# Optimization experiments

Hardware: AMD Instinct MI355X
Metric: run time of the kernel (lower is better)

Reference implementation:

```python
import jax, jax.numpy as jnp
import numpy as np

H, W = 48, 48
MAXDIM = 1


def _build_complex(Hh, Ww):
    # Regular grid triangulation (each cell split along its anti-diagonal),
    # matching scipy Delaunay on a grid up to arbitrary diagonal tie-breaking.
    r, c = np.meshgrid(np.arange(Hh), np.arange(Ww), indexing="ij")
    v = (r * Ww + c).astype(np.int32)
    he = np.stack([v[:, :-1].ravel(), v[:, 1:].ravel()], 1)      # horizontal
    ve = np.stack([v[:-1, :].ravel(), v[1:, :].ravel()], 1)      # vertical
    de = np.stack([v[:-1, 1:].ravel(), v[1:, :-1].ravel()], 1)   # anti-diagonal (v01,v10)
    edges = np.concatenate([he, ve, de], 0).astype(np.int32)
    nh, nv = he.shape[0], ve.shape[0]
    he_id = lambda rr, cc: rr * (Ww - 1) + cc
    ve_id = lambda rr, cc: nh + rr * Ww + cc
    de_id = lambda rr, cc: nh + nv + rr * (Ww - 1) + cc
    rr, cc = np.meshgrid(np.arange(Hh - 1), np.arange(Ww - 1), indexing="ij")
    rr, cc = rr.ravel(), cc.ravel()
    triA = np.stack([he_id(rr, cc), ve_id(rr, cc), de_id(rr, cc)], 1)
    triB = np.stack([de_id(rr, cc), ve_id(rr, cc + 1), he_id(rr + 1, cc)], 1)
    tri_edges = np.concatenate([triA, triB], 0).astype(np.int32)
    return edges, tri_edges


def setup_inputs() -> dict:
    key = jax.random.key(0)
    img = jax.random.normal(key, (H, W), dtype=jnp.float32)
    edges, tri_edges = _build_complex(H, W)
    return {"img": img, "edges": jnp.asarray(edges), "tri_edges": jnp.asarray(tri_edges)}


def _filtration(img, edges, tri_edges):
    # Sublevel-set filtration: simplex value = max over its vertices.
    f = img.reshape(-1)
    fe = jnp.max(f[edges], axis=1)          # (E,)
    ft = jnp.max(fe[tri_edges], axis=1)     # (F,) max of edge maxes == max of vertices
    return jnp.concatenate([f, fe, ft])     # (m,)


@jax.jit
def _pairing(vals, edges, tri_edges):
    # Standard persistence boundary-matrix reduction over Z/2.
    E, F = edges.shape[0], tri_edges.shape[0]
    m = vals.shape[0]
    N = m - E - F
    dims = jnp.concatenate([jnp.zeros(N, jnp.int32), jnp.ones(E, jnp.int32), jnp.full((F,), 2, jnp.int32)])
    order = jnp.lexsort((dims, vals))                  # value-primary, dim tiebreak -> faces before cofaces
    rank = jnp.zeros(m, jnp.int32).at[order].set(jnp.arange(m, dtype=jnp.int32))
    R = jnp.zeros((m, m), dtype=bool)
    ecol = rank[N + jnp.arange(E)]
    R = R.at[rank[edges[:, 0]], ecol].set(True).at[rank[edges[:, 1]], ecol].set(True)
    tcol = rank[N + E + jnp.arange(F)]
    for k in range(3):
        R = R.at[rank[N + tri_edges[:, k]], tcol].set(True)
    idx = jnp.arange(m, dtype=jnp.int32)
    low = lambda col: jnp.max(jnp.where(col, idx, -1))

    def body(j, state):
        Rm, piv = state
        def cond(s):
            Rr, p = s
            l = low(Rr[:, j])
            return (l >= 0) & (p[l] >= 0)
        def step(s):
            Rr, p = s
            l = low(Rr[:, j])
            return Rr.at[:, j].set(Rr[:, j] ^ Rr[:, p[l]]), p
        Rm, piv = jax.lax.while_loop(cond, step, (Rm, piv))
        l = low(Rm[:, j])
        piv = jax.lax.cond(l >= 0, lambda p: p.at[l].set(jnp.int32(j)), lambda p: p, piv)
        return Rm, piv

    R, piv = jax.lax.fori_loop(0, m, body, (R, -jnp.ones(m, jnp.int32)))
    lowR = jnp.max(jnp.where(R, idx[:, None], -1), axis=0)
    return order, piv, lowR, dims[order]


def _diagrams(vals, order, pivot, lowR, dims_sorted, maxdim):
    vs = vals[order]
    fmax = jnp.max(vals)                      # finite death for essential classes
    paired = pivot >= 0                       # rows that are paired births
    death_paired = vs[jnp.clip(pivot, 0)]
    essential = (lowR < 0) & (pivot < 0)      # positive, never killed
    dgms = []
    for d in range(maxdim + 1):
        pd = paired & (dims_sorted == d)
        ed = essential & (dims_sorted == d)
        birth = jnp.where(pd | ed, vs, 0.0)
        death = jnp.where(pd, death_paired, 0.0) + jnp.where(ed, fmax, 0.0)
        dgms.append(jnp.stack([birth, death], axis=-1))
    return jnp.stack(dgms)                    # (maxdim+1, m, 2), zero-padded


def reference(img, edges, tri_edges):
    vals = _filtration(img, edges, tri_edges)
    order, pivot, lowR, dims_sorted = _pairing(vals, edges, tri_edges)
    return _diagrams(vals, order, pivot, lowR, dims_sorted, MAXDIM)
```

## Files before the change

kernel.cpp:

```cpp
#include <hip/hip_runtime.h>
#include <stdint.h>
#include <math.h>

typedef unsigned long long u64;

#define FMAXC 4418
#define KRANGES 128
#define BLK 1024
#define TSZ 1024
#define PSTR 1056

static __device__ __forceinline__ uint32_t f2ord(float f) {
  uint32_t u = __float_as_uint(f);
  return (u & 0x80000000u) ? ~u : (u | 0x80000000u);
}

static __device__ __forceinline__ u64 shfl_xor_u64(u64 x, int msk) {
  int lo = __shfl_xor((int)(uint32_t)x, msk, 64);
  int hi = __shfl_xor((int)(uint32_t)(x >> 32), msk, 64);
  return ((u64)(uint32_t)hi << 32) | (uint32_t)lo;
}

static __device__ __forceinline__ void edge_ab(int e, int W, int nh, int nv,
                                               int* a, int* b) {
  if (e < nh) {
    int r = e / (W - 1), c = e - r * (W - 1);
    *a = r * W + c; *b = *a + 1;
  } else if (e < nh + nv) {
    int q = e - nh;
    int r = q / W, c = q - r * W;
    *a = r * W + c; *b = *a + W;
  } else {
    int q = e - nh - nv;
    int r = q / (W - 1), c = q - r * (W - 1);
    *a = r * W + c + 1; *b = (r + 1) * W + c;
  }
}

static __device__ __forceinline__ void edge_tri(int e, int W, int H, int nh, int nv,
                                                int FH, int* tA, int* tB) {
  if (e < nh) {
    int r = e / (W - 1), c = e - r * (W - 1);
    *tA = (r <= H - 2) ? r * (W - 1) + c : -1;
    *tB = (r >= 1) ? FH + (r - 1) * (W - 1) + c : -1;
  } else if (e < nh + nv) {
    int q = e - nh;
    int r = q / W, c = q - r * W;
    *tA = (c <= W - 2) ? r * (W - 1) + c : -1;
    *tB = (c >= 1) ? FH + r * (W - 1) + (c - 1) : -1;
  } else {
    int q = e - nh - nv;
    int r = q / (W - 1), c = q - r * (W - 1);
    *tA = r * (W - 1) + c;
    *tB = FH + r * (W - 1) + c;
  }
}

static __device__ __forceinline__ int rep(volatile int* par, int v) {
  int p = par[v];
  if (p == v) return v;
  int gp = par[p];
  while (p != gp) {
    par[v] = gp;
    v = p; p = gp; gp = par[p];
  }
  return p;
}

static __device__ __forceinline__ void hook(volatile int* vp, uint32_t ab) {
  int va = (int)(ab >> 16), vb = (int)(ab & 0xffffu);
  int pa = vp[va], pb = vp[vb];
  int ga = vp[pa], gb = vp[pb];
  while (pa != ga || pb != gb) {
    if (pa != ga) { vp[va] = ga; va = pa; pa = ga; ga = vp[pa]; }
    if (pb != gb) { vp[vb] = gb; vb = pb; pb = gb; gb = vp[pb]; }
  }
  int u = pa, w = pb;
  while (u != w) {
    if (u < w) { int t = u; u = w; w = t; }
    int old = atomicCAS((int*)&vp[u], u, w);
    if (old == u) break;
    u = rep(vp, old);
    w = rep(vp, w);
  }
}

__global__ __launch_bounds__(BLK) void k_prep(
    const float* img, float* vals, u64* keys, u64* tilesorted, uint32_t* pfx,
    uint32_t* pack, float* out, int N, int E, int F, int m, int W, int H,
    int nh, int nv, int FH, int out_n, int NT) {
  __shared__ __align__(16) u64 s[TSZ];
  __shared__ uint32_t wsum[16];
  int tid = threadIdx.x, bid = blockIdx.x;
  int lane = tid & 63, wid = tid >> 6;
  int gi = bid * BLK + tid;
  for (int i = gi; i < out_n; i += NT * BLK) out[i] = 0.0f;
  if (gi < m) pack[gi] = 0u;
  int base = bid * TSZ;
  int lim = min(TSZ, m - base);
  u64 v = ~0ull;
  if (gi < m) {
    float val;
    int i = gi;
    if (i < N) {
      val = img[i];
    } else if (i < N + E) {
      int a, b;
      edge_ab(i - N, W, nh, nv, &a, &b);
      val = fmaxf(img[a], img[b]);
    } else {
      int t = i - N - E;
      if (t < FH) {
        int r = t / (W - 1), c = t - r * (W - 1);
        int bse = r * W + c;
        val = fmaxf(img[bse], fmaxf(img[bse + 1], img[bse + W]));
      } else {
        int q = t - FH;
        int r = q / (W - 1), c = q - r * (W - 1);
        int bse = r * W + c;
        val = fmaxf(img[bse + 1], fmaxf(img[bse + W], img[bse + W + 1]));
      }
    }
    vals[i] = val;
    v = ((u64)f2ord(val) << 32) | (u64)(uint32_t)i;
    keys[i] = v;
  }
  for (int k = 2; k <= TSZ; k <<= 1) {
    for (int j = k >> 1; j > 0; j >>= 1) {
      bool asc = ((tid & k) == 0);
      if (j >= 64) {
        s[tid] = v;
        __syncthreads();
        u64 u = s[tid ^ j];
        bool takeMin = (((tid & j) == 0) == asc);
        v = takeMin ? (v < u ? v : u) : (v > u ? v : u);
        __syncthreads();
      } else {
        u64 u = shfl_xor_u64(v, j);
        bool takeMin = (((tid & j) == 0) == asc);
        v = takeMin ? (v < u ? v : u) : (v > u ? v : u);
      }
    }
  }
  tilesorted[base + tid] = v;
  uint32_t v0 = 0;
  if (tid < lim) {
    int idx = (int)(v & 0xffffffffu);
    v0 = (idx < N) ? 1u : (idx < N + E ? (1u << 16) : 0u);
  }
  uint32_t sv = v0;
  #pragma unroll
  for (int off = 1; off < 64; off <<= 1) {
    uint32_t t = (uint32_t)__shfl_up((int)sv, off, 64);
    if (lane >= off) sv += t;
  }
  if (lane == 63) wsum[wid] = sv;
  __syncthreads();
  if (tid < 16) {
    uint32_t t = wsum[tid];
    #pragma unroll
    for (int off = 1; off < 16; off <<= 1) {
      uint32_t u2 = (uint32_t)__shfl_up((int)t, off, 64);
      if (tid >= off) t += u2;
    }
    wsum[tid] = t;
  }
  __syncthreads();
  uint32_t incl = sv + (wid > 0 ? wsum[wid - 1] : 0u);
  pfx[bid * PSTR + tid] = incl - v0;
  if (tid == TSZ - 1) pfx[bid * PSTR + TSZ] = incl;
}

__global__ __launch_bounds__(BLK) void k_count(
    const u64* keys, const u64* ts, const uint32_t* pfx, uint32_t* pack,
    int N, int E, int m) {
  __shared__ __align__(16) u64 s[TSZ];
  __shared__ uint32_t sp[TSZ + 1];
  int tid = threadIdx.x;
  int t = blockIdx.x;
  s[tid] = ts[(t << 10) + tid];
  sp[tid] = pfx[t * PSTR + tid];
  if (tid == 0) sp[TSZ] = pfx[t * PSTR + TSZ];
  __syncthreads();
  int ki = blockIdx.y * BLK + tid;
  if (ki >= m) return;
  u64 k0 = keys[ki];
  int cls0 = (ki < N) ? 0 : (ki < N + E ? 1 : 2);
  int lo = 0;
  #pragma unroll
  for (int step = TSZ >> 1; step >= 1; step >>= 1) {
    if (s[lo + step - 1] < k0) lo += step;
  }
  lo += (s[lo] < k0) ? 1 : 0;
  uint32_t p = sp[lo];
  uint32_t c0 = p & 0xffffu, c1 = p >> 16;
  uint32_t cc = (cls0 == 0) ? c0 : (cls0 == 1 ? c1 : (uint32_t)lo - c0 - c1);
  atomicAdd(&pack[ki], (cc << 16) | (uint32_t)lo);
}

__global__ __launch_bounds__(256) void k_maps(
    const uint32_t* pack, const float* vals,
    float* vsorted, int* vr_to_rank, int* er_to_rank, int* noderank1,
    uint32_t* eAB0, uint32_t* eAB1,
    int N, int E, int F, int m, int W, int H, int nh, int nv, int FH) {
  int i = blockIdx.x * blockDim.x + threadIdx.x;
  if (i >= m) return;
  uint32_t pk = pack[i];
  int rank = (int)(pk & 0xffffu);
  int cls = (int)(pk >> 16);
  vsorted[rank] = vals[i];
  if (i < N) {
    vr_to_rank[cls] = rank;
  } else if (i < N + E) {
    int e = i - N, er = cls;
    er_to_rank[er] = rank;
    int a, b;
    edge_ab(e, W, nh, nv, &a, &b);
    uint32_t va = pack[a] >> 16, vb = pack[b] >> 16;
    eAB0[er] = (va << 16) | vb;
    int tA, tB;
    edge_tri(e, W, H, nh, nv, FH, &tA, &tB);
    uint32_t na = (tA >= 0) ? ((uint32_t)F - (pack[N + E + tA] >> 16)) : 0u;
    uint32_t nb = (tB >= 0) ? ((uint32_t)F - (pack[N + E + tB] >> 16)) : 0u;
    eAB1[E - 1 - er] = (na << 16) | nb;
  } else {
    noderank1[F - cls] = rank;
  }
}

__global__ __launch_bounds__(BLK) void k_pair(
    const uint32_t* eAB0, const uint32_t* eAB1,
    const int* vr_to_rank, const int* er_to_rank, const int* noderank1,
    const float* vsorted, float* out, int N, int E, int F, int C, int m) {
  __shared__ __align__(16) int s_par[2 * (FMAXC + 1)];
  __shared__ uint32_t s_rc[64];
  __shared__ int s_ci[64];
  __shared__ int2 s_pairs[64];
  __shared__ int s_cnt[2];
  int tid = threadIdx.x, bid = blockIdx.x;
  int g = bid >> 7;
  int r = bid & (KRANGES - 1);
  int NODES = (g == 0) ? N : (F + 1);
  const uint32_t* eAB = (g == 0) ? eAB0 : eAB1;
  int P = r * C;
  if (P >= E) return;
  int hi = min(P + C, E);
  int nR = hi - P;
  int n1 = (nR + 1) >> 1;
  int n2 = nR - n1;
  int Q = P + n1;
  int* par1 = s_par;
  int* par2 = s_par + (FMAXC + 1);
  volatile int* vp1 = par1;
  volatile int* vp2 = par2;
  for (int x = tid; x < NODES; x += BLK) par1[x] = x;
  __syncthreads();
  for (int i = tid; i < P; i += BLK) hook(vp1, eAB[i]);
  __syncthreads();
  for (int x = tid; x < NODES; x += BLK) {
    int r0 = x;
    while (vp1[r0] != r0) r0 = vp1[r0];
    par1[x] = r0;
  }
  __syncthreads();
  for (int x = tid; x < NODES; x += BLK) par2[x] = par1[x];
  __syncthreads();
  for (int i = tid; i < n1; i += BLK) hook(vp2, eAB[P + i]);
  __syncthreads();
  for (int x = tid; x < NODES; x += BLK) {
    int r0 = x;
    while (vp2[r0] != r0) r0 = vp2[r0];
    par2[x] = r0;
  }
  __syncthreads();
  for (int q = tid; q < nR; q += BLK) {
    int sub = (q >= n1);
    int qq = sub ? q - n1 : q;
    uint32_t ab = eAB[(sub ? Q : P) + qq];
    const int* par = sub ? par2 : par1;
    int ra = par[ab >> 16], rb = par[ab & 0xffffu];
    s_rc[sub * 32 + qq] = ((uint32_t)ra << 16) | (uint32_t)rb;
  }
  __syncthreads();
  if (tid < 128) {
    int sub = tid >> 6;
    int lane = tid & 63;
    int nC = sub ? n2 : n1;
    int ebase = sub ? Q : P;
    uint32_t* rc = s_rc + sub * 32;
    int* ci = s_ci + sub * 32;
    int* par = sub ? par2 : par1;
    uint32_t rr = (lane < nC) ? rc[lane] : 0u;
    int keep = (lane < nC) && ((rr >> 16) != (rr & 0xffffu));
    u64 mask = __ballot(keep);
    if (keep) {
      int idx = __popcll(mask & ((1ull << lane) - 1ull));
      rc[idx] = rr;
      ci[idx] = lane;
    }
    int kc = __popcll(mask);
    if (lane == 0) {
      int c = 0;
      for (int i = 0; i < kc; ++i) {
        uint32_t rr2 = rc[i];
        int x = (int)(rr2 >> 16), y = (int)(rr2 & 0xffffu);
        while (par[x] != x) { par[x] = par[par[x]]; x = par[x]; }
        while (par[y] != y) { par[y] = par[par[y]]; y = par[y]; }
        if (x != y) {
          int die = x > y ? x : y, sur = x < y ? x : y;
          par[die] = sur;
          s_pairs[sub * 32 + c] = make_int2(die, ebase + ci[i]);
          c++;
        }
      }
      s_cnt[sub] = c;
    }
  }
  __syncthreads();
  int c0 = s_cnt[0], c1 = s_cnt[1];
  if (g == 0) {
    for (int q = tid; q < c0 + c1; q += BLK) {
      int2 pq = s_pairs[q < c0 ? q : 32 + (q - c0)];
      int b = vr_to_rank[pq.x], d = er_to_rank[pq.y];
      out[2 * b] = vsorted[b];
      out[2 * b + 1] = vsorted[d];
    }
    if (r == 0 && tid == 0) {
      out[0] = vsorted[0];
      out[1] = vsorted[m - 1];
    }
  } else {
    float* o1 = out + 2 * (size_t)m;
    for (int q = tid; q < c0 + c1; q += BLK) {
      int2 pq = s_pairs[q < c0 ? q : 32 + (q - c0)];
      int er = E - 1 - pq.y;
      int b = er_to_rank[er], d = noderank1[pq.x];
      o1[2 * b] = vsorted[b];
      o1[2 * b + 1] = vsorted[d];
    }
  }
}

extern "C" void kernel_launch(void* const* d_in, const int* in_sizes, int n_in,
                              void* d_out, int out_size, void* d_ws, size_t ws_size,
                              hipStream_t stream) {
  const float* img = (const float*)d_in[0];
  int N = in_sizes[0];
  int E = in_sizes[1] / 2;
  int F = in_sizes[2] / 3;
  int m = N + E + F;
  int C = (E + KRANGES - 1) / KRANGES;
  int W = (int)(sqrt((double)N) + 0.5);
  int H = N / W;
  int nh = H * (W - 1);
  int nv = (H - 1) * W;
  int FH = (H - 1) * (W - 1);
  int NT = (m + TSZ - 1) / TSZ;
  float* out = (float*)d_out;

  char* p = (char*)d_ws;
  auto alloc = [&](size_t bytes) { char* r = p; p += (bytes + 255) & ~(size_t)255; return r; };
  u64* keys        = (u64*)alloc((size_t)NT * TSZ * 8);
  u64* tilesorted  = (u64*)alloc((size_t)NT * TSZ * 8);
  uint32_t* pfx    = (uint32_t*)alloc((size_t)NT * PSTR * 4);
  float* vals      = (float*)alloc((size_t)m * 4);
  float* vsorted   = (float*)alloc((size_t)m * 4);
  uint32_t* pack   = (uint32_t*)alloc((size_t)m * 4);
  int* vr_to_rank  = (int*)alloc((size_t)N * 4);
  int* er_to_rank  = (int*)alloc((size_t)E * 4);
  int* noderank1   = (int*)alloc((size_t)(F + 1) * 4);
  uint32_t* eAB0   = (uint32_t*)alloc((size_t)E * 4);
  uint32_t* eAB1   = (uint32_t*)alloc((size_t)E * 4);
  (void)ws_size; (void)n_in;

  k_prep<<<NT, BLK, 0, stream>>>(img, vals, keys, tilesorted, pfx, pack, out,
                                 N, E, F, m, W, H, nh, nv, FH, out_size, NT);
  dim3 cg(NT, NT);
  k_count<<<cg, BLK, 0, stream>>>(keys, tilesorted, pfx, pack, N, E, m);
  k_maps<<<(m + 255) / 256, 256, 0, stream>>>(pack, vals, vsorted,
                                              vr_to_rank, er_to_rank, noderank1,
                                              eAB0, eAB1, N, E, F, m, W, H, nh, nv, FH);
  k_pair<<<2 * KRANGES, BLK, 0, stream>>>(eAB0, eAB1, vr_to_rank, er_to_rank,
                                          noderank1, vsorted, out, N, E, F, C, m);
}
```

Measured before the change: 45.67 us.

## Double the pairing blocks with single union-find per block; double-buffer sort smem

The pairing kernel previously split each of 128 edge ranges into two halves within one block, which needed two union-find arrays. It now launches 256 ranges, one per block, each using a single shared union-find array. Each block still rebuilds the prefix forest from scratch, so total redundant hooking work roughly doubles while per-block shared memory halves. The bitonic tile sort also gains a double-buffered shared array, which drops one barrier per shared-memory step, and a barrier is added before the warp-sum write.

Result: no change. 45.26 us, median of 2 (-0.9%).

```diff
diff --git a/kernel.cpp b/kernel.cpp
--- a/kernel.cpp
+++ b/kernel.cpp
@@ -5,7 +5,7 @@
 typedef unsigned long long u64;
 
 #define FMAXC 4418
-#define KRANGES 128
+#define KRANGES 256
 #define BLK 1024
 #define TSZ 1024
 #define PSTR 1056
@@ -89,7 +89,7 @@
     const float* img, float* vals, u64* keys, u64* tilesorted, uint32_t* pfx,
     uint32_t* pack, float* out, int N, int E, int F, int m, int W, int H,
     int nh, int nv, int FH, int out_n, int NT) {
-  __shared__ __align__(16) u64 s[TSZ];
+  __shared__ __align__(16) u64 s[2][TSZ];
   __shared__ uint32_t wsum[16];
   int tid = threadIdx.x, bid = blockIdx.x;
   int lane = tid & 63, wid = tid >> 6;
@@ -125,21 +125,21 @@
     v = ((u64)f2ord(val) << 32) | (u64)(uint32_t)i;
     keys[i] = v;
   }
+  int cur = 0;
   for (int k = 2; k <= TSZ; k <<= 1) {
     for (int j = k >> 1; j > 0; j >>= 1) {
       bool asc = ((tid & k) == 0);
+      bool takeMin = (((tid & j) == 0) == asc);
+      u64 u;
       if (j >= 64) {
-        s[tid] = v;
+        s[cur][tid] = v;
         __syncthreads();
-        u64 u = s[tid ^ j];
-        bool takeMin = (((tid & j) == 0) == asc);
-        v = takeMin ? (v < u ? v : u) : (v > u ? v : u);
-        __syncthreads();
+        u = s[cur][tid ^ j];
+        cur ^= 1;
       } else {
-        u64 u = shfl_xor_u64(v, j);
-        bool takeMin = (((tid & j) == 0) == asc);
-        v = takeMin ? (v < u ? v : u) : (v > u ? v : u);
+        u = shfl_xor_u64(v, j);
       }
+      v = takeMin ? (v < u ? v : u) : (v > u ? v : u);
     }
   }
   tilesorted[base + tid] = v;
@@ -154,6 +154,7 @@
     uint32_t t = (uint32_t)__shfl_up((int)sv, off, 64);
     if (lane >= off) sv += t;
   }
+  __syncthreads();
   if (lane == 63) wsum[wid] = sv;
   __syncthreads();
   if (tid < 16) {
@@ -232,13 +233,13 @@
     const uint32_t* eAB0, const uint32_t* eAB1,
     const int* vr_to_rank, const int* er_to_rank, const int* noderank1,
     const float* vsorted, float* out, int N, int E, int F, int C, int m) {
-  __shared__ __align__(16) int s_par[2 * (FMAXC + 1)];
+  __shared__ __align__(16) int s_par[FMAXC + 1];
   __shared__ uint32_t s_rc[64];
   __shared__ int s_ci[64];
   __shared__ int2 s_pairs[64];
-  __shared__ int s_cnt[2];
+  __shared__ int s_cnt;
   int tid = threadIdx.x, bid = blockIdx.x;
-  int g = bid >> 7;
+  int g = bid >> 8;
   int r = bid & (KRANGES - 1);
   int NODES = (g == 0) ? N : (F + 1);
   const uint32_t* eAB = (g == 0) ? eAB0 : eAB1;
@@ -246,81 +247,54 @@
   if (P >= E) return;
   int hi = min(P + C, E);
   int nR = hi - P;
-  int n1 = (nR + 1) >> 1;
-  int n2 = nR - n1;
-  int Q = P + n1;
-  int* par1 = s_par;
-  int* par2 = s_par + (FMAXC + 1);
-  volatile int* vp1 = par1;
-  volatile int* vp2 = par2;
-  for (int x = tid; x < NODES; x += BLK) par1[x] = x;
-  __syncthreads();
-  for (int i = tid; i < P; i += BLK) hook(vp1, eAB[i]);
+  volatile int* vp = s_par;
+  for (int x = tid; x < NODES; x += BLK) s_par[x] = x;
+  __syncthreads();
+  for (int i = tid; i < P; i += BLK) hook(vp, eAB[i]);
   __syncthreads();
   for (int x = tid; x < NODES; x += BLK) {
     int r0 = x;
-    while (vp1[r0] != r0) r0 = vp1[r0];
-    par1[x] = r0;
-  }
-  __syncthreads();
-  for (int x = tid; x < NODES; x += BLK) par2[x] = par1[x];
-  __syncthreads();
-  for (int i = tid; i < n1; i += BLK) hook(vp2, eAB[P + i]);
-  __syncthreads();
-  for (int x = tid; x < NODES; x += BLK) {
-    int r0 = x;
-    while (vp2[r0] != r0) r0 = vp2[r0];
-    par2[x] = r0;
+    while (vp[r0] != r0) r0 = vp[r0];
+    s_par[x] = r0;
   }
   __syncthreads();
   for (int q = tid; q < nR; q += BLK) {
-    int sub = (q >= n1);
-    int qq = sub ? q - n1 : q;
-    uint32_t ab = eAB[(sub ? Q : P) + qq];
-    const int* par = sub ? par2 : par1;
-    int ra = par[ab >> 16], rb = par[ab & 0xffffu];
-    s_rc[sub * 32 + qq] = ((uint32_t)ra << 16) | (uint32_t)rb;
-  }
-  __syncthreads();
-  if (tid < 128) {
-    int sub = tid >> 6;
-    int lane = tid & 63;
-    int nC = sub ? n2 : n1;
-    int ebase = sub ? Q : P;
-    uint32_t* rc = s_rc + sub * 32;
-    int* ci = s_ci + sub * 32;
-    int* par = sub ? par2 : par1;
-    uint32_t rr = (lane < nC) ? rc[lane] : 0u;
-    int keep = (lane < nC) && ((rr >> 16) != (rr & 0xffffu));
+    uint32_t ab = eAB[P + q];
+    int ra = s_par[ab >> 16], rb = s_par[ab & 0xffffu];
+    s_rc[q] = ((uint32_t)ra << 16) | (uint32_t)rb;
+  }
+  __syncthreads();
+  if (tid < 64) {
+    uint32_t rr = (tid < nR) ? s_rc[tid] : 0u;
+    int keep = (tid < nR) && ((rr >> 16) != (rr & 0xffffu));
     u64 mask = __ballot(keep);
     if (keep) {
-      int idx = __popcll(mask & ((1ull << lane) - 1ull));
-      rc[idx] = rr;
-      ci[idx] = lane;
+      int idx = __popcll(mask & ((1ull << tid) - 1ull));
+      s_rc[idx] = rr;
+      s_ci[idx] = tid;
     }
     int kc = __popcll(mask);
-    if (lane == 0) {
+    if (tid == 0) {
       int c = 0;
       for (int i = 0; i < kc; ++i) {
-        uint32_t rr2 = rc[i];
+        uint32_t rr2 = s_rc[i];
         int x = (int)(rr2 >> 16), y = (int)(rr2 & 0xffffu);
-        while (par[x] != x) { par[x] = par[par[x]]; x = par[x]; }
-        while (par[y] != y) { par[y] = par[par[y]]; y = par[y]; }
+        while (s_par[x] != x) { s_par[x] = s_par[s_par[x]]; x = s_par[x]; }
+        while (s_par[y] != y) { s_par[y] = s_par[s_par[y]]; y = s_par[y]; }
         if (x != y) {
           int die = x > y ? x : y, sur = x < y ? x : y;
-          par[die] = sur;
-          s_pairs[sub * 32 + c] = make_int2(die, ebase + ci[i]);
-          c++;
+          s_par[die] = sur;
+          s_pairs[c++] = make_int2(die, P + s_ci[i]);
         }
       }
-      s_cnt[sub] = c;
-    }
-  }
-  __syncthreads();
-  int c0 = s_cnt[0], c1 = s_cnt[1];
+      s_cnt = c;
+    }
+  }
+  __syncthreads();
+  int c = s_cnt;
   if (g == 0) {
-    for (int q = tid; q < c0 + c1; q += BLK) {
-      int2 pq = s_pairs[q < c0 ? q : 32 + (q - c0)];
+    for (int q = tid; q < c; q += BLK) {
+      int2 pq = s_pairs[q];
       int b = vr_to_rank[pq.x], d = er_to_rank[pq.y];
       out[2 * b] = vsorted[b];
       out[2 * b + 1] = vsorted[d];
@@ -331,8 +305,8 @@
     }
   } else {
     float* o1 = out + 2 * (size_t)m;
-    for (int q = tid; q < c0 + c1; q += BLK) {
-      int2 pq = s_pairs[q < c0 ? q : 32 + (q - c0)];
+    for (int q = tid; q < c; q += BLK) {
+      int2 pq = s_pairs[q];
       int er = E - 1 - pq.y;
       int b = er_to_rank[er], d = noderank1[pq.x];
       o1[2 * b] = vsorted[b];
```
